# Performance work log

Measured on AMD Instinct MI355X. Metric: run time of the kernel, lower is better.

The kernel has to match this reference:

```python
import jax, jax.numpy as jnp
import numpy as np

B, F, T = 64, 256, 1024  # batch, input features, time steps
H, O = 1024, 512         # hidden units, output projection dim


def setup_inputs() -> dict:
    key = jax.random.key(0)
    k = jax.random.split(key, 4)
    scale_x = 1.0 / np.sqrt(F)
    scale_h = 1.0 / np.sqrt(H)
    return {
        "x": jax.random.normal(k[0], (B, F, T), dtype=jnp.float32),
        "Wx": jax.random.normal(k[1], (F, H), dtype=jnp.float32) * scale_x,
        "Wh": jax.random.normal(k[2], (H, H), dtype=jnp.float32) * scale_h,
        "b": jnp.zeros((H,), dtype=jnp.float32),
        "Wout": jax.random.normal(k[3], (H, O), dtype=jnp.float32) * scale_h,
        "bout": jnp.zeros((O,), dtype=jnp.float32),
    }


def reference(x, Wx, Wh, b, Wout, bout):
    # inputs are (B, F, T); tf.unstack(axis=-1) -> per-step (B, F) slices
    xT = jnp.moveaxis(x, -1, 0)  # (T, B, F)
    s0 = jnp.zeros((x.shape[0], Wh.shape[0]), dtype=x.dtype)

    def step(state, xt):
        # simple RNN cell: tanh(x@Wx + s@Wh + b)
        new_state = jnp.tanh(xt @ Wx + state @ Wh + b)
        return new_state, new_state

    _, states = jax.lax.scan(step, s0, xT)       # (T, B, H)
    states = jnp.moveaxis(states, 0, 1)          # (B, T, H) -- tf.stack(axis=1)
    out = states @ Wout + bout                   # per-timestep Dense projection
    return out
```

## Files before the change

### kernel.cpp

```cpp
#include <hip/hip_runtime.h>
#include <math.h>

#define B_ 64
#define F_ 256
#define T_ 1024
#define H_ 1024
#define O_ 512

#define RG_ 4
#define CG_ 16
#define NWG (RG_ * CG_)

#define S3_T 65536

typedef short short8 __attribute__((ext_vector_type(8)));
typedef float f32x4 __attribute__((ext_vector_type(4)));
typedef unsigned int uint2v __attribute__((ext_vector_type(2)));
typedef unsigned int uint4v __attribute__((ext_vector_type(4)));

__device__ inline float bf2f(unsigned short u) {
    union { unsigned int i; float f; } v; v.i = ((unsigned int)u) << 16; return v.f;
}
__device__ inline unsigned short f2bf(float f) {
    union { float f; unsigned int i; } v; v.f = f;
    unsigned int i = v.i;
    unsigned int r = (i + 0x7fffu + ((i >> 16) & 1u)) >> 16;
    return (unsigned short)r;
}

__global__ void wt_transpose(const float* __restrict__ src,
                             unsigned short* __restrict__ dst, int K, int N) {
    __shared__ float tile[32][33];
    int n0 = blockIdx.x * 32, k0 = blockIdx.y * 32;
    int tx = threadIdx.x, ty = threadIdx.y;
    for (int i = ty; i < 32; i += 8)
        tile[i][tx] = src[(size_t)(k0 + i) * N + n0 + tx];
    __syncthreads();
    for (int i = ty; i < 32; i += 8)
        dst[(size_t)(n0 + i) * K + k0 + tx] = f2bf(tile[tx][i]);
}

__global__ void xpose_x(const float* __restrict__ x, unsigned short* __restrict__ xT) {
    __shared__ float tile[64][65];
    int id = blockIdx.x;
    int b = id >> 6;
    int ft = (id >> 4) & 3;
    int tt = id & 15;
    int f0 = ft * 64, t0 = tt * 64;
    for (int i = threadIdx.x; i < 64 * 64; i += 256) {
        int fl = i >> 6, tl = i & 63;
        tile[fl][tl] = x[((size_t)(b * F_ + f0 + fl)) * T_ + t0 + tl];
    }
    __syncthreads();
    for (int i = threadIdx.x; i < 64 * 64; i += 256) {
        int tl = i >> 6, fl = i & 63;
        xT[((size_t)(t0 + tl) * B_ + b) * F_ + f0 + fl] = f2bf(tile[fl][tl]);
    }
}

__global__ __launch_bounds__(256) void proj_kernel(
    const unsigned short* __restrict__ xT, const unsigned short* __restrict__ WxT,
    const float* __restrict__ bias, unsigned short* __restrict__ S) {
    int nb = blockIdx.x;
    int mb = blockIdx.y;
    int wave = threadIdx.x >> 6, lane = threadIdx.x & 63;
    int col16 = lane & 15, quad = lane >> 4;
    int m0 = mb * 64 + wave * 16;
    int n0 = nb * 64;

    f32x4 acc[4];
    for (int s = 0; s < 4; ++s)
        for (int r = 0; r < 4; ++r) acc[s][r] = 0.0f;

    #pragma unroll
    for (int kc = 0; kc < F_ / 32; ++kc) {
        int k0 = kc * 32 + quad * 8;
        short8 a = *reinterpret_cast<const short8*>(xT + (size_t)(m0 + col16) * F_ + k0);
        #pragma unroll
        for (int s = 0; s < 4; ++s) {
            short8 bfr = *reinterpret_cast<const short8*>(
                WxT + (size_t)(n0 + s * 16 + col16) * F_ + k0);
            acc[s] = __builtin_amdgcn_mfma_f32_16x16x32_bf16(a, bfr, acc[s], 0, 0, 0);
        }
    }
    #pragma unroll
    for (int s = 0; s < 4; ++s) {
        int col = n0 + s * 16 + col16;
        float bb = bias[col];
        #pragma unroll
        for (int r = 0; r < 4; ++r) {
            int brow = wave * 16 + quad * 4 + r;
            size_t off = (size_t)mb * S3_T + (size_t)(brow >> 4) * 16384 +
                         (size_t)(col >> 6) * 1024 + (brow & 15) * 64 + (col & 63);
            S[off] = f2bf(acc[s][r] + bb);
        }
    }
}

__global__ void init_flags(unsigned int* flags) {
    if (threadIdx.x < NWG) flags[threadIdx.x * 16] = 0;
}

__global__ __launch_bounds__(256, 1) void rnn_persistent(
    unsigned short* __restrict__ S, const unsigned short* __restrict__ WhT,
    unsigned int* flags) {
    const int bid = blockIdx.x;
    const int rg = bid >> 4;
    const int cg = bid & 15;
    const int tid = threadIdx.x;
    const int wave = tid >> 6, lane = tid & 63;
    const int col16 = lane & 15, quad = lane >> 4;

    __shared__ unsigned short Atile[16 * 1024];

    unsigned int* myflag = &flags[(rg * 16 + cg) * 16];

    {
        unsigned short* St0 = S + (size_t)rg * 16384 + (size_t)cg * 1024;
        const unsigned short* sp = St0 + tid * 4;
        unsigned short h0 = f2bf(tanhf(bf2f(sp[0])));
        unsigned short h1 = f2bf(tanhf(bf2f(sp[1])));
        unsigned short h2 = f2bf(tanhf(bf2f(sp[2])));
        unsigned short h3 = f2bf(tanhf(bf2f(sp[3])));
        uint2v pk;
        pk[0] = (unsigned int)h0 | ((unsigned int)h1 << 16);
        pk[1] = (unsigned int)h2 | ((unsigned int)h3 << 16);
        asm volatile("global_store_dwordx2 %0, %1, off sc0 sc1"
                     :: "v"((unsigned long long)(uintptr_t)(St0 + tid * 4)), "v"(pk)
                     : "memory");
    }
    asm volatile("s_waitcnt vmcnt(0)" ::: "memory");
    __syncthreads();
    if (tid == 0)
        __hip_atomic_store(myflag, 1u, __ATOMIC_RELAXED, __HIP_MEMORY_SCOPE_AGENT);

    int dead = 0;

    for (int t = 1; t < T_; ++t) {
        unsigned short* Stb = S + (size_t)t * S3_T + (size_t)rg * 16384 + (size_t)cg * 1024;
        const unsigned short* Ablk = S + (size_t)(t - 1) * S3_T + (size_t)rg * 16384;

        float xp[4];
        #pragma unroll
        for (int r = 0; r < 4; ++r)
            xp[r] = bf2f(Stb[(quad * 4 + r) * 64 + wave * 16 + col16]);

        if (wave == 0 && !dead) {
            const unsigned tgt = (unsigned)t;
            int guard = 0;
            while (true) {
                unsigned v = __hip_atomic_load(&flags[(rg * 16 + (lane & 15)) * 16],
                                               __ATOMIC_RELAXED, __HIP_MEMORY_SCOPE_AGENT);
                if (__ballot(v >= tgt) == ~0ull) break;
                __builtin_amdgcn_s_sleep(1);
                if (++guard > (1 << 16)) { dead = 1; break; }
            }
        }
        asm volatile("" ::: "memory");
        __syncthreads();

        uint4v av[8];
        #pragma unroll
        for (int i = 0; i < 8; ++i) {
            int kblk = i * 16 + (tid >> 4);
            int m = tid & 15;
            const unsigned short* gp = Ablk + ((kblk >> 3) * 1024 + m * 64 + (kblk & 7) * 8);
            asm volatile("global_load_dwordx4 %0, %1, off sc0 sc1"
                         : "=v"(av[i])
                         : "v"((unsigned long long)(uintptr_t)gp));
        }
        asm volatile("s_waitcnt vmcnt(0)" ::: "memory");
        __builtin_amdgcn_sched_barrier(0);
        #pragma unroll
        for (int i = 0; i < 8; ++i) {
            int kblk = i * 16 + (tid >> 4);
            int m = tid & 15;
            int l16 = (kblk >> 2) * 64 + (kblk & 3) * 16 + m;
            *reinterpret_cast<uint4v*>(&Atile[l16 * 8]) = av[i];
        }
        __syncthreads();

        f32x4 acc0 = {0.f, 0.f, 0.f, 0.f};
        f32x4 acc1 = {0.f, 0.f, 0.f, 0.f};
        const int nglob = cg * 64 + wave * 16 + col16;
        const unsigned short* Brow = WhT + (size_t)nglob * 1024 + quad * 8;
        const unsigned short* Abase = Atile + quad * 128 + col16 * 8;
        #pragma unroll
        for (int kc = 0; kc < 32; kc += 2) {
            short8 a0 = *reinterpret_cast<const short8*>(Abase + kc * 512);
            short8 a1 = *reinterpret_cast<const short8*>(Abase + (kc + 1) * 512);
            short8 b0 = *reinterpret_cast<const short8*>(Brow + kc * 32);
            short8 b1 = *reinterpret_cast<const short8*>(Brow + (kc + 1) * 32);
            acc0 = __builtin_amdgcn_mfma_f32_16x16x32_bf16(a0, b0, acc0, 0, 0, 0);
            acc1 = __builtin_amdgcn_mfma_f32_16x16x32_bf16(a1, b1, acc1, 0, 0, 0);
        }

        #pragma unroll
        for (int r = 0; r < 4; ++r) {
            float h = tanhf(xp[r] + acc0[r] + acc1[r]);
            unsigned int hv = (unsigned int)f2bf(h);
            unsigned short* dp = Stb + (quad * 4 + r) * 64 + wave * 16 + col16;
            asm volatile("global_store_short %0, %1, off sc0 sc1"
                         :: "v"((unsigned long long)(uintptr_t)dp), "v"(hv)
                         : "memory");
        }
        asm volatile("s_waitcnt vmcnt(0)" ::: "memory");
        __syncthreads();
        if (tid == 0)
            __hip_atomic_store(myflag, (unsigned)(t + 1), __ATOMIC_RELAXED,
                               __HIP_MEMORY_SCOPE_AGENT);
    }
}

__global__ __launch_bounds__(256) void out_kernel(
    const unsigned short* __restrict__ S, const unsigned short* __restrict__ WoutT,
    const float* __restrict__ bout, float* __restrict__ out) {
    int nb = blockIdx.x;
    int tt = blockIdx.y;
    int wave = threadIdx.x >> 6, lane = threadIdx.x & 63;
    int col16 = lane & 15, quad = lane >> 4;
    int n0 = nb * 64;

    f32x4 acc[4];
    for (int s = 0; s < 4; ++s)
        for (int r = 0; r < 4; ++r) acc[s][r] = 0.0f;

    const unsigned short* arow =
        S + (size_t)tt * S3_T + (size_t)wave * 16384 + (size_t)col16 * 64 + quad * 8;

    #pragma unroll 4
    for (int kc = 0; kc < H_ / 32; ++kc) {
        int k0 = kc * 32 + quad * 8;
        short8 a = *reinterpret_cast<const short8*>(arow + (kc >> 1) * 1024 + (kc & 1) * 32);
        #pragma unroll
        for (int s = 0; s < 4; ++s) {
            short8 bfr = *reinterpret_cast<const short8*>(
                WoutT + (size_t)(n0 + s * 16 + col16) * H_ + k0);
            acc[s] = __builtin_amdgcn_mfma_f32_16x16x32_bf16(a, bfr, acc[s], 0, 0, 0);
        }
    }
    #pragma unroll
    for (int s = 0; s < 4; ++s) {
        int col = n0 + s * 16 + col16;
        float bo = bout[col];
        #pragma unroll
        for (int r = 0; r < 4; ++r) {
            int bidx = wave * 16 + quad * 4 + r;
            out[((size_t)bidx * T_ + tt) * O_ + col] = acc[s][r] + bo;
        }
    }
}

extern "C" void kernel_launch(void* const* d_in, const int* in_sizes, int n_in,
                              void* d_out, int out_size, void* d_ws, size_t ws_size,
                              hipStream_t stream) {
    const float* x    = (const float*)d_in[0];
    const float* Wx   = (const float*)d_in[1];
    const float* Wh   = (const float*)d_in[2];
    const float* bias = (const float*)d_in[3];
    const float* Wout = (const float*)d_in[4];
    const float* bout = (const float*)d_in[5];
    float* out = (float*)d_out;

    unsigned short* WhT   = (unsigned short*)d_ws;
    unsigned short* WxT   = WhT + (size_t)H_ * H_;
    unsigned short* WoutT = WxT + (size_t)H_ * F_;
    unsigned short* S     = WoutT + (size_t)O_ * H_;
    unsigned short* xT    = (unsigned short*)d_out;
    unsigned int* flags   = (unsigned int*)((char*)d_out + (32u << 20));

    wt_transpose<<<dim3(H_ / 32, H_ / 32), dim3(32, 8), 0, stream>>>(Wh, WhT, H_, H_);
    wt_transpose<<<dim3(H_ / 32, F_ / 32), dim3(32, 8), 0, stream>>>(Wx, WxT, F_, H_);
    wt_transpose<<<dim3(O_ / 32, H_ / 32), dim3(32, 8), 0, stream>>>(Wout, WoutT, H_, O_);
    xpose_x<<<dim3(4096), dim3(256), 0, stream>>>(x, xT);
    init_flags<<<1, 64, 0, stream>>>(flags);

    proj_kernel<<<dim3(16, 1024), dim3(256), 0, stream>>>(xT, WxT, bias, S);

    rnn_persistent<<<dim3(NWG), dim3(256), 0, stream>>>(S, WhT, flags);

    out_kernel<<<dim3(8, 1024), dim3(256), 0, stream>>>(S, WoutT, bout, out);
}
```

Baseline: 7.522 ms.

## Keep Wh slice in LDS and co-locate each RNN chain on one XCD for local sync

Each workgroup now caches its 64-column slice of Wh^T in shared memory once, so B operands no longer come from global memory every step. The launch grows to 128 blocks and chains are mapped with bid&7, aiming to place each independent 16-block batch chain on a single XCD, which is detected at runtime via HW_REG_XCC_ID. When co-location is confirmed, flags and state use L2-local atomics and plain stores instead of system-coherent sc0/sc1 traffic. A fallback path keeps the uncached protocol. The risks are the dependence on the hardware block-to-XCD scheduling and the 128KB LDS footprint per block.

New measurement: 6.626 ms. -11.9%, faster.

```diff
diff --git a/kernel.cpp b/kernel.cpp
--- a/kernel.cpp
+++ b/kernel.cpp
@@ -7,16 +7,15 @@
 #define H_ 1024
 #define O_ 512
 
-#define RG_ 4
-#define CG_ 16
-#define NWG (RG_ * CG_)
+#define NCHAIN 4
+#define NMEM   16
 
 #define S3_T 65536
 
 typedef short short8 __attribute__((ext_vector_type(8)));
 typedef float f32x4 __attribute__((ext_vector_type(4)));
-typedef unsigned int uint2v __attribute__((ext_vector_type(2)));
 typedef unsigned int uint4v __attribute__((ext_vector_type(4)));
+typedef unsigned long long ull;
 
 __device__ inline float bf2f(unsigned short u) {
     union { unsigned int i; float f; } v; v.i = ((unsigned int)u) << 16; return v.f;
@@ -97,119 +96,197 @@
     }
 }
 
-__global__ void init_flags(unsigned int* flags) {
-    if (threadIdx.x < NWG) flags[threadIdx.x * 16] = 0;
+__global__ void init_ctrl(unsigned int* ctrl) {
+    for (int i = threadIdx.x; i < 8192; i += 256) ctrl[i] = 0u;
+}
+
+template<bool LOCAL>
+__device__ __forceinline__ void st_h(unsigned short* p, unsigned short v) {
+    if (LOCAL) {
+        *p = v;
+    } else {
+        asm volatile("global_store_short %0, %1, off sc0 sc1"
+                     :: "v"((ull)(uintptr_t)p), "v"((unsigned int)v) : "memory");
+    }
+}
+
+template<bool LOCAL>
+__device__ __forceinline__ void flag_store(unsigned int* p, unsigned int v) {
+    if (LOCAL) {
+        asm volatile("global_atomic_swap %0, %1, off"
+                     :: "v"((ull)(uintptr_t)p), "v"(v) : "memory");
+    } else {
+        __hip_atomic_store(p, v, __ATOMIC_RELAXED, __HIP_MEMORY_SCOPE_AGENT);
+    }
+}
+
+template<bool LOCAL>
+__device__ __forceinline__ unsigned int flag_load(unsigned int* p) {
+    unsigned int old;
+    if (LOCAL) {
+        asm volatile("global_atomic_add %0, %1, %2, off sc0\n\t"
+                     "s_waitcnt vmcnt(0)"
+                     : "=v"(old) : "v"((ull)(uintptr_t)p), "v"(0u) : "memory");
+    } else {
+        old = __hip_atomic_load(p, __ATOMIC_RELAXED, __HIP_MEMORY_SCOPE_AGENT);
+    }
+    return old;
+}
+
+template<bool LOCAL>
+__device__ void rnn_loop(unsigned short* S, const unsigned short* Bs,
+                         unsigned int* ctrl, int chain, int m, int tid) {
+    const int wave = tid >> 6, lane = tid & 63;
+    const int col16 = lane & 15, quad = lane >> 4;
+    unsigned int* myflag = &ctrl[(chain * 16 + m) * 32];
+
+    {
+        unsigned short* St0 = S + (size_t)chain * 16384 + (size_t)m * 1024;
+        #pragma unroll
+        for (int i = 0; i < 4; ++i) {
+            int e = tid * 4 + i;
+            st_h<LOCAL>(&St0[e], f2bf(tanhf(bf2f(St0[e]))));
+        }
+    }
+    asm volatile("s_waitcnt vmcnt(0)" ::: "memory");
+    __syncthreads();
+    if (tid == 0) flag_store<LOCAL>(myflag, 1u);
+
+    int dead = 0;
+
+    for (int t = 1; t < T_; ++t) {
+        unsigned short* Stb = S + (size_t)t * S3_T + (size_t)chain * 16384 + (size_t)m * 1024;
+        const unsigned short* Ab = S + (size_t)(t - 1) * S3_T + (size_t)chain * 16384;
+
+        float xp[4];
+        #pragma unroll
+        for (int r = 0; r < 4; ++r)
+            xp[r] = bf2f(Stb[(quad * 4 + r) * 64 + wave * 16 + col16]);
+        asm volatile("s_waitcnt vmcnt(0)" ::: "memory");
+
+        if (wave == 0 && !dead) {
+            const unsigned int tgt = (unsigned int)t;
+            int g = 0;
+            while (true) {
+                unsigned int v = flag_load<LOCAL>(&ctrl[(chain * 16 + (lane & 15)) * 32]);
+                if (__ballot(v >= tgt) == ~0ull) break;
+                if (!LOCAL) __builtin_amdgcn_s_sleep(1);
+                if (++g > (1 << 17)) { dead = 1; break; }
+            }
+        }
+        __syncthreads();
+
+        f32x4 acc0 = {0.f, 0.f, 0.f, 0.f};
+        f32x4 acc1 = {0.f, 0.f, 0.f, 0.f};
+        const unsigned short* Arow  = Ab + col16 * 64 + quad * 8;
+        const unsigned short* Bslab = Bs + wave * 16384 + quad * 128 + col16 * 8;
+        if (LOCAL) {
+            #pragma unroll
+            for (int kc2 = 0; kc2 < 16; ++kc2) {
+                short8 a0 = *reinterpret_cast<const short8*>(Arow + kc2 * 1024);
+                short8 a1 = *reinterpret_cast<const short8*>(Arow + kc2 * 1024 + 32);
+                short8 b0 = *reinterpret_cast<const short8*>(Bslab + (2 * kc2) * 512);
+                short8 b1 = *reinterpret_cast<const short8*>(Bslab + (2 * kc2 + 1) * 512);
+                acc0 = __builtin_amdgcn_mfma_f32_16x16x32_bf16(a0, b0, acc0, 0, 0, 0);
+                acc1 = __builtin_amdgcn_mfma_f32_16x16x32_bf16(a1, b1, acc1, 0, 0, 0);
+            }
+        } else {
+            for (int kc2 = 0; kc2 < 16; ++kc2) {
+                short8 a0, a1;
+                ull p0 = (ull)(uintptr_t)(Arow + kc2 * 1024);
+                ull p1 = p0 + 64;
+                asm volatile("global_load_dwordx4 %0, %2, off sc0 sc1\n\t"
+                             "global_load_dwordx4 %1, %3, off sc0 sc1\n\t"
+                             "s_waitcnt vmcnt(0)"
+                             : "=v"(a0), "=v"(a1) : "v"(p0), "v"(p1) : "memory");
+                __builtin_amdgcn_sched_barrier(0);
+                short8 b0 = *reinterpret_cast<const short8*>(Bslab + (2 * kc2) * 512);
+                short8 b1 = *reinterpret_cast<const short8*>(Bslab + (2 * kc2 + 1) * 512);
+                acc0 = __builtin_amdgcn_mfma_f32_16x16x32_bf16(a0, b0, acc0, 0, 0, 0);
+                acc1 = __builtin_amdgcn_mfma_f32_16x16x32_bf16(a1, b1, acc1, 0, 0, 0);
+            }
+        }
+
+        #pragma unroll
+        for (int r = 0; r < 4; ++r) {
+            float h = tanhf(xp[r] + acc0[r] + acc1[r]);
+            st_h<LOCAL>(Stb + (quad * 4 + r) * 64 + wave * 16 + col16, f2bf(h));
+        }
+        asm volatile("s_waitcnt vmcnt(0)" ::: "memory");
+        __syncthreads();
+        if (tid == 0) flag_store<LOCAL>(myflag, (unsigned int)(t + 1));
+    }
 }
 
 __global__ __launch_bounds__(256, 1) void rnn_persistent(
     unsigned short* __restrict__ S, const unsigned short* __restrict__ WhT,
-    unsigned int* flags) {
+    unsigned int* ctrl) {
     const int bid = blockIdx.x;
-    const int rg = bid >> 4;
-    const int cg = bid & 15;
+    if ((bid & 7) >= NCHAIN) return;
+    const int chain = bid & 7;
+    const int m = bid >> 3;
     const int tid = threadIdx.x;
     const int wave = tid >> 6, lane = tid & 63;
-    const int col16 = lane & 15, quad = lane >> 4;
-
-    __shared__ unsigned short Atile[16 * 1024];
-
-    unsigned int* myflag = &flags[(rg * 16 + cg) * 16];
+    const int w = chain * 16 + m;
+
+    __shared__ unsigned short Bs[64 * 1024];
+    __shared__ int s_proto;
 
     {
-        unsigned short* St0 = S + (size_t)rg * 16384 + (size_t)cg * 1024;
-        const unsigned short* sp = St0 + tid * 4;
-        unsigned short h0 = f2bf(tanhf(bf2f(sp[0])));
-        unsigned short h1 = f2bf(tanhf(bf2f(sp[1])));
-        unsigned short h2 = f2bf(tanhf(bf2f(sp[2])));
-        unsigned short h3 = f2bf(tanhf(bf2f(sp[3])));
-        uint2v pk;
-        pk[0] = (unsigned int)h0 | ((unsigned int)h1 << 16);
-        pk[1] = (unsigned int)h2 | ((unsigned int)h3 << 16);
-        asm volatile("global_store_dwordx2 %0, %1, off sc0 sc1"
-                     :: "v"((unsigned long long)(uintptr_t)(St0 + tid * 4)), "v"(pk)
-                     : "memory");
-    }
-    asm volatile("s_waitcnt vmcnt(0)" ::: "memory");
-    __syncthreads();
-    if (tid == 0)
-        __hip_atomic_store(myflag, 1u, __ATOMIC_RELAXED, __HIP_MEMORY_SCOPE_AGENT);
-
-    int dead = 0;
-
-    for (int t = 1; t < T_; ++t) {
-        unsigned short* Stb = S + (size_t)t * S3_T + (size_t)rg * 16384 + (size_t)cg * 1024;
-        const unsigned short* Ablk = S + (size_t)(t - 1) * S3_T + (size_t)rg * 16384;
-
-        float xp[4];
-        #pragma unroll
-        for (int r = 0; r < 4; ++r)
-            xp[r] = bf2f(Stb[(quad * 4 + r) * 64 + wave * 16 + col16]);
-
-        if (wave == 0 && !dead) {
-            const unsigned tgt = (unsigned)t;
-            int guard = 0;
-            while (true) {
-                unsigned v = __hip_atomic_load(&flags[(rg * 16 + (lane & 15)) * 16],
-                                               __ATOMIC_RELAXED, __HIP_MEMORY_SCOPE_AGENT);
-                if (__ballot(v >= tgt) == ~0ull) break;
-                __builtin_amdgcn_s_sleep(1);
-                if (++guard > (1 << 16)) { dead = 1; break; }
-            }
-        }
-        asm volatile("" ::: "memory");
-        __syncthreads();
-
-        uint4v av[8];
-        #pragma unroll
-        for (int i = 0; i < 8; ++i) {
-            int kblk = i * 16 + (tid >> 4);
-            int m = tid & 15;
-            const unsigned short* gp = Ablk + ((kblk >> 3) * 1024 + m * 64 + (kblk & 7) * 8);
-            asm volatile("global_load_dwordx4 %0, %1, off sc0 sc1"
-                         : "=v"(av[i])
-                         : "v"((unsigned long long)(uintptr_t)gp));
-        }
+        const int n0 = m * 64;
+        for (int i = tid; i < 8192; i += 256) {
+            int c = i >> 7, j = i & 127;
+            int kc = j >> 2, q = j & 3;
+            int dst = (c >> 4) * 16384 + kc * 512 + q * 128 + (c & 15) * 8;
+            *reinterpret_cast<uint4v*>(&Bs[dst]) =
+                *reinterpret_cast<const uint4v*>(WhT + (size_t)(n0 + c) * 1024 + j * 8);
+        }
+    }
+
+    unsigned int* flags = ctrl;
+    unsigned int* ready = &ctrl[2048];
+    unsigned int* xcds  = &ctrl[2560];
+    unsigned int* toks  = &ctrl[5120];
+
+    unsigned int xcd = 0;
+    asm volatile("s_getreg_b32 %0, hwreg(HW_REG_XCC_ID)" : "=s"(xcd));
+    if (tid == 0) {
+        toks[w * 32] = (unsigned int)(w + 1);
         asm volatile("s_waitcnt vmcnt(0)" ::: "memory");
-        __builtin_amdgcn_sched_barrier(0);
-        #pragma unroll
-        for (int i = 0; i < 8; ++i) {
-            int kblk = i * 16 + (tid >> 4);
-            int m = tid & 15;
-            int l16 = (kblk >> 2) * 64 + (kblk & 3) * 16 + m;
-            *reinterpret_cast<uint4v*>(&Atile[l16 * 8]) = av[i];
-        }
-        __syncthreads();
-
-        f32x4 acc0 = {0.f, 0.f, 0.f, 0.f};
-        f32x4 acc1 = {0.f, 0.f, 0.f, 0.f};
-        const int nglob = cg * 64 + wave * 16 + col16;
-        const unsigned short* Brow = WhT + (size_t)nglob * 1024 + quad * 8;
-        const unsigned short* Abase = Atile + quad * 128 + col16 * 8;
-        #pragma unroll
-        for (int kc = 0; kc < 32; kc += 2) {
-            short8 a0 = *reinterpret_cast<const short8*>(Abase + kc * 512);
-            short8 a1 = *reinterpret_cast<const short8*>(Abase + (kc + 1) * 512);
-            short8 b0 = *reinterpret_cast<const short8*>(Brow + kc * 32);
-            short8 b1 = *reinterpret_cast<const short8*>(Brow + (kc + 1) * 32);
-            acc0 = __builtin_amdgcn_mfma_f32_16x16x32_bf16(a0, b0, acc0, 0, 0, 0);
-            acc1 = __builtin_amdgcn_mfma_f32_16x16x32_bf16(a1, b1, acc1, 0, 0, 0);
-        }
-
-        #pragma unroll
-        for (int r = 0; r < 4; ++r) {
-            float h = tanhf(xp[r] + acc0[r] + acc1[r]);
-            unsigned int hv = (unsigned int)f2bf(h);
-            unsigned short* dp = Stb + (quad * 4 + r) * 64 + wave * 16 + col16;
-            asm volatile("global_store_short %0, %1, off sc0 sc1"
-                         :: "v"((unsigned long long)(uintptr_t)dp), "v"(hv)
-                         : "memory");
-        }
-        asm volatile("s_waitcnt vmcnt(0)" ::: "memory");
-        __syncthreads();
-        if (tid == 0)
-            __hip_atomic_store(myflag, (unsigned)(t + 1), __ATOMIC_RELAXED,
-                               __HIP_MEMORY_SCOPE_AGENT);
-    }
+        __hip_atomic_store(&xcds[w * 32], xcd + 1u, __ATOMIC_RELAXED,
+                           __HIP_MEMORY_SCOPE_AGENT);
+        __hip_atomic_fetch_add(ready, 1u, __ATOMIC_RELEASE, __HIP_MEMORY_SCOPE_AGENT);
+    }
+    __syncthreads();
+
+    if (tid == 0) {
+        int g = 0, got = 0;
+        while (true) {
+            unsigned int v = __hip_atomic_load(ready, __ATOMIC_RELAXED,
+                                               __HIP_MEMORY_SCOPE_AGENT);
+            if (v >= 64u) { got = 1; break; }
+            __builtin_amdgcn_s_sleep(2);
+            if (++g > (1 << 20)) break;
+        }
+        s_proto = got ? -1 : 0;
+    }
+    __syncthreads();
+
+    if (wave == 0) {
+        int mm = lane & 15;
+        unsigned int xv = __hip_atomic_load(&xcds[(chain * 16 + mm) * 32],
+                                            __ATOMIC_RELAXED, __HIP_MEMORY_SCOPE_AGENT);
+        unsigned int tv = toks[(chain * 16 + mm) * 32];
+        unsigned int x0 = __shfl(xv, 0);
+        bool uni = (__ballot(xv == x0) == ~0ull) && (x0 != 0u);
+        bool tok = (__ballot(tv == (unsigned int)(chain * 16 + mm + 1)) == ~0ull);
+        if (lane == 0) s_proto = (s_proto != 0 && uni && tok) ? 1 : 0;
+    }
+    __syncthreads();
+    const int local_ok = s_proto;
+
+    if (local_ok) rnn_loop<true>(S, Bs, ctrl, chain, m, tid);
+    else          rnn_loop<false>(S, Bs, ctrl, chain, m, tid);
 }
 
 __global__ __launch_bounds__(256) void out_kernel(
@@ -267,17 +344,17 @@
     unsigned short* WoutT = WxT + (size_t)H_ * F_;
     unsigned short* S     = WoutT + (size_t)O_ * H_;
     unsigned short* xT    = (unsigned short*)d_out;
-    unsigned int* flags   = (unsigned int*)((char*)d_out + (32u << 20));
+    unsigned int* ctrl    = (unsigned int*)((char*)d_out + (32u << 20));
 
     wt_transpose<<<dim3(H_ / 32, H_ / 32), dim3(32, 8), 0, stream>>>(Wh, WhT, H_, H_);
     wt_transpose<<<dim3(H_ / 32, F_ / 32), dim3(32, 8), 0, stream>>>(Wx, WxT, F_, H_);
     wt_transpose<<<dim3(O_ / 32, H_ / 32), dim3(32, 8), 0, stream>>>(Wout, WoutT, H_, O_);
     xpose_x<<<dim3(4096), dim3(256), 0, stream>>>(x, xT);
-    init_flags<<<1, 64, 0, stream>>>(flags);
+    init_ctrl<<<1, 256, 0, stream>>>(ctrl);
 
     proj_kernel<<<dim3(16, 1024), dim3(256), 0, stream>>>(xT, WxT, bias, S);
 
-    rnn_persistent<<<dim3(NWG), dim3(256), 0, stream>>>(S, WhT, flags);
+    rnn_persistent<<<dim3(128), dim3(256), 0, stream>>>(S, WhT, ctrl);
 
     out_kernel<<<dim3(8, 1024), dim3(256), 0, stream>>>(S, WoutT, bout, out);
 }
```
